# Optimization experiments

Hardware: AMD Instinct MI355X
Metric: run time of the kernel (lower is better)

The kernel has to match this reference:

```python
import jax, jax.numpy as jnp
import numpy as np
from jax import lax

# dims: B=16, T=1500, E(enc)=512, D(dec)=512, A(att_dim)=512, C(out_channels)=10, K(kernel)=201, H(heads)=4
SHARPENING = 1.0


def setup_inputs() -> dict:
    key = jax.random.key(0)
    ks = jax.random.split(key, 12)
    B, T, E, D, A, C, K, H = 16, 1500, 512, 512, 512, 10, 201, 4
    s = 0.02
    return {
        "enc_out": jax.random.normal(ks[0], (B, T, E), dtype=jnp.float32),
        "x_lens": jax.random.randint(ks[1], (B,), 1, T + 1, dtype=jnp.int32),
        "dec_out": jax.random.normal(ks[2], (B, 1, D), dtype=jnp.float32),
        "aw_step": jax.random.uniform(ks[3], (B, T, H), dtype=jnp.float32),
        "W_enc": jax.random.normal(ks[4], (H, E, A), dtype=jnp.float32) * s,
        "b_enc": jnp.zeros((H, A), dtype=jnp.float32),
        "W_dec": jax.random.normal(ks[5], (H, D, A), dtype=jnp.float32) * s,
        "W_conv": jax.random.normal(ks[6], (H, C, A), dtype=jnp.float32) * s,
        "conv_w": jax.random.normal(ks[7], (H, C, K), dtype=jnp.float32) * s,
        "v": jax.random.normal(ks[8], (H, A), dtype=jnp.float32) * s,
        "W_mha": jax.random.normal(ks[9], (H * E, E), dtype=jnp.float32) * s,
        "b_mha": jnp.zeros((E,), dtype=jnp.float32),
    }


def reference(enc_out, x_lens, dec_out, aw_step, W_enc, b_enc, W_dec, W_conv, conv_w, v, W_mha, b_mha):
    B, T, E = enc_out.shape
    H, C, K = conv_w.shape
    # per-head encoder projection (cached enc_out_a in original): [B,T,H,A]
    enc_a = jnp.einsum('bte,hea->btha', enc_out, W_enc) + b_enc
    # per-head decoder projection, broadcast over T: [B,1,H,A]
    dec_a = jnp.einsum('bqd,hda->bqha', dec_out, W_dec)
    # location features: per-head 1D conv over T of previous attention weights
    lhs = jnp.transpose(aw_step, (0, 2, 1))          # [B,H,T]
    rhs = conv_w.reshape(H * C, 1, K)                # grouped conv, one group per head
    conv = lax.conv_general_dilated(lhs, rhs, (1,), 'SAME',
                                    dimension_numbers=('NCH', 'OIH', 'NCH'),
                                    feature_group_count=H)  # [B,H*C,T]
    conv = conv.reshape(B, H, C, T)
    conv_a = jnp.einsum('bhct,hca->btha', conv, W_conv)      # [B,T,H,A]
    # additive energy: v^T tanh(enc + dec + conv) per head -> [B,T,H]
    energy = jnp.einsum('btha,ha->bth', jnp.tanh(enc_a + dec_a + conv_a), v)
    # original multiplies energy by 0/1 mask (NOT -inf) before softmax over T
    mask = (jnp.arange(T)[None, :] < x_lens[:, None]).astype(energy.dtype)  # [B,T]
    energy = energy * mask[:, :, None] * SHARPENING
    aw = jax.nn.softmax(energy, axis=1)                      # softmax over T per head
    # per-head context, heads concatenated along feature dim: [B,1,H*E]
    ctx = jnp.einsum('bte,bth->bhe', enc_out, aw).reshape(B, 1, H * E)
    context_vec = ctx @ W_mha + b_mha                        # [B,1,E]
    return context_vec, aw
```

## Files before the change

### kernel.cpp

```cpp
#include <hip/hip_runtime.h>
#include <hip/hip_bf16.h>

#define B_ 16
#define T_ 1500
#define E_ 512
#define A_ 512
#define H_ 4
#define C_ 10
#define K_ 201
#define M_ (B_*T_)
#define KW_ 544

typedef __attribute__((ext_vector_type(8))) short short8v;
typedef __attribute__((ext_vector_type(4))) float f32x4;
typedef __attribute__((ext_vector_type(4))) unsigned short ushort4v;
typedef __attribute__((ext_vector_type(8))) unsigned short ushort8v;

typedef __attribute__((address_space(1))) const char gch;
typedef __attribute__((address_space(3))) char lch;

__device__ __forceinline__ void gload16(const void* g, void* l) {
    __builtin_amdgcn_global_load_lds((gch*)g, (lch*)l, 16, 0, 0);
}

__device__ inline unsigned short f2bf(float x) {
    unsigned int u = __float_as_uint(x);
    return (unsigned short)((u + 0x7fffu + ((u >> 16) & 1u)) >> 16);
}

__global__ void k_prep(const float* __restrict__ enc, unsigned short* __restrict__ encB,
                       const float* __restrict__ Wenc, const float* __restrict__ Wconv,
                       unsigned short* __restrict__ WencTp,
                       const float* __restrict__ dec, const float* __restrict__ Wdec,
                       const float* __restrict__ benc, float* __restrict__ decA,
                       float* __restrict__ out,
                       const float* __restrict__ aw_step, const float* __restrict__ conv_w,
                       unsigned short* __restrict__ convA, float* __restrict__ wszero) {
    __shared__ float smemf[4456];
    int bid = blockIdx.x;
    int tid = threadIdx.x;

    if (bid < 6000) {
        int i = bid * 256 + tid;
        const float4* src = (const float4*)enc + (size_t)i * 2;
        float4 f0 = src[0], f1 = src[1];
        ushort8v o = { f2bf(f0.x), f2bf(f0.y), f2bf(f0.z), f2bf(f0.w),
                       f2bf(f1.x), f2bf(f1.y), f2bf(f1.z), f2bf(f1.w) };
        *(ushort8v*)&encB[(size_t)i * 8] = o;
        return;
    }
    if (bid < 7088) {
        int idx = bid - 6000;
        int bx = idx & 15, by = (idx >> 4) % 17, h = idx / 272;
        int tx = tid & 31, ty = tid >> 5;
        if (by == 16) {
            int base = (h * 16 + bx) * 1024;
            #pragma unroll
            for (int k = 0; k < 4; k++) {
                int i2 = base + k * 256 + tid;
                int c = i2 & 31, n = (i2 >> 5) & 511, hh = i2 >> 14;
                float val = (c < C_) ? Wconv[(hh * C_ + c) * A_ + n] : 0.0f;
                WencTp[((size_t)(hh * A_ + n)) * KW_ + 512 + c] = f2bf(val);
            }
            return;
        }
        float (*tile)[33] = (float(*)[33])smemf;
        int e0 = bx * 32, a0 = by * 32;
        const float* src = Wenc + h * E_ * A_;
        #pragma unroll
        for (int i = 0; i < 4; i++) tile[ty + i*8][tx] = src[(e0 + ty + i*8) * A_ + a0 + tx];
        __syncthreads();
        unsigned short* dst = WencTp + (size_t)h * A_ * KW_;
        #pragma unroll
        for (int i = 0; i < 4; i++) dst[(size_t)(a0 + ty + i*8) * KW_ + e0 + tx] = f2bf(tile[tx][ty + i*8]);
        return;
    }
    if (bid < 7152) {
        int bh = bid - 7088, b = bh >> 2, h = bh & 3;
        int a = tid;
        if (bh < 32) out[bh * 256 + a] = 0.0f;
        float acc0 = 0.f, acc1 = 0.f;
        const float* W = Wdec + h * E_ * A_;
        const float* x = dec + b * 512;
        for (int d = 0; d < 512; d++) {
            float s = x[d];
            acc0 += s * W[d * A_ + a];
            acc1 += s * W[d * A_ + a + 256];
        }
        decA[bh * A_ + a]       = acc0 + benc[h * A_ + a];
        decA[bh * A_ + a + 256] = acc1 + benc[h * A_ + a + 256];
        return;
    }
    {
        int i = bid - 7152;
        int b = i & 15, h = (i >> 4) & 3, tc = i >> 6;
        int t0 = tc * 250;
        float* seg = smemf;
        unsigned short* outl = (unsigned short*)(smemf + 456);
        {
            int idx = (i * 256 + tid) * 2;
            if (idx < 128768)     wszero[idx] = 0.0f;
            if (idx + 1 < 128768) wszero[idx + 1] = 0.0f;
        }
        for (int idx = tid; idx < 450; idx += 256) {
            int tt = t0 - 100 + idx;
            seg[idx] = (tt >= 0 && tt < T_) ? aw_step[(b * T_ + tt) * H_ + h] : 0.0f;
        }
        for (int idx = tid; idx < 8000; idx += 256) outl[idx] = 0;
        __syncthreads();
        if (tid < 250) {
            float acc[10] = {0,0,0,0,0,0,0,0,0,0};
            const float* cw = conv_w + h * C_ * K_;
            for (int k = 0; k < K_; k++) {
                float sv = seg[tid + k];
                #pragma unroll
                for (int c = 0; c < 10; c++) acc[c] += sv * cw[c * K_ + k];
            }
            #pragma unroll
            for (int c = 0; c < 10; c++) outl[tid * 32 + c] = f2bf(acc[c]);
        }
        __syncthreads();
        unsigned short* dst = convA + ((size_t)h * M_ + (size_t)b * T_ + t0) * 32;
        for (int idx = tid; idx < 2000; idx += 256)
            *(ushort4v*)&dst[idx * 4] = *(const ushort4v*)&outl[idx * 4];
    }
}

__launch_bounds__(256)
__global__ void k_energy(const unsigned short* __restrict__ encB,
                         const unsigned short* __restrict__ WencTp,
                         const unsigned short* __restrict__ convA,
                         const float* __restrict__ decA,
                         const float* __restrict__ v,
                         float* __restrict__ energy) {
    __shared__ unsigned short As[2][4096];
    __shared__ unsigned short Bs[2][4096];
    int m0 = blockIdx.x * 128;
    int h  = blockIdx.y >> 2;
    int n0 = (blockIdx.y & 3) * 128;
    int tid = threadIdx.x;
    int lane = tid & 63, w = tid >> 6;
    int wr = w >> 1, wc = w & 1;
    int lc = lane & 15, lr16 = lane >> 4;

    int srow  = lane >> 2;
    int sslot = (lane & 3) ^ ((lane >> 3) & 3);

    const char* pa[2]; const char* pb[2]; const char* pca[2];
    #pragma unroll
    for (int i = 0; i < 2; i++) {
        int c = i * 4 + w;
        int row = c * 16 + srow;
        int grow = min(m0 + row, M_ - 1);
        pa[i]  = (const char*)encB + ((size_t)grow * 512 + sslot * 8) * 2;
        pb[i]  = (const char*)WencTp + ((size_t)(h * 512 + n0 + row) * KW_ + sslot * 8) * 2;
        pca[i] = (const char*)convA + (((size_t)h * M_ + grow) * 32 + sslot * 8) * 2;
    }

    int kslot = (lr16 ^ ((lc >> 1) & 3)) * 8;

    f32x4 acc[4][4] = {};

    #pragma unroll
    for (int i = 0; i < 2; i++) {
        int c = i * 4 + w;
        gload16(pa[i], (char*)As[0] + c * 1024);
        gload16(pb[i], (char*)Bs[0] + c * 1024);
    }

    for (int s = 0; s < 17; ++s) {
        const int buf = s & 1;
        if (s < 15) {
            #pragma unroll
            for (int i = 0; i < 2; i++) {
                int c = i * 4 + w;
                gload16(pa[i] + (s + 1) * 64, (char*)As[buf ^ 1] + c * 1024);
                gload16(pb[i] + (s + 1) * 64, (char*)Bs[buf ^ 1] + c * 1024);
            }
            asm volatile("s_waitcnt vmcnt(4)" ::: "memory");
        } else if (s == 15) {
            #pragma unroll
            for (int i = 0; i < 2; i++) {
                int c = i * 4 + w;
                gload16(pca[i], (char*)As[buf ^ 1] + c * 1024);
                gload16(pb[i] + 16 * 64, (char*)Bs[buf ^ 1] + c * 1024);
            }
            asm volatile("s_waitcnt vmcnt(4)" ::: "memory");
        } else {
            asm volatile("s_waitcnt vmcnt(0)" ::: "memory");
        }
        __builtin_amdgcn_s_barrier();
        __builtin_amdgcn_sched_barrier(0);
        {
            short8v a[4], b[4];
            #pragma unroll
            for (int mi = 0; mi < 4; mi++)
                a[mi] = *(const short8v*)&As[buf][(wr * 64 + mi * 16 + lc) * 32 + kslot];
            #pragma unroll
            for (int ni = 0; ni < 4; ni++)
                b[ni] = *(const short8v*)&Bs[buf][(wc * 64 + ni * 16 + lc) * 32 + kslot];
            #pragma unroll
            for (int mi = 0; mi < 4; mi++)
                #pragma unroll
                for (int ni = 0; ni < 4; ni++)
                    acc[mi][ni] = __builtin_amdgcn_mfma_f32_16x16x32_bf16(a[mi], b[ni], acc[mi][ni], 0, 0, 0);
        }
        __builtin_amdgcn_sched_barrier(0);
        __builtin_amdgcn_s_barrier();
    }

    #pragma unroll
    for (int mi = 0; mi < 4; mi++) {
        #pragma unroll
        for (int r = 0; r < 4; r++) {
            int mrow = m0 + wr * 64 + mi * 16 + lr16 * 4 + r;
            if (mrow < M_) {
                int bb = mrow / 1500;
                const float* dA = decA + (bb * 4 + h) * 512;
                float s = 0.f;
                #pragma unroll
                for (int ni = 0; ni < 4; ni++) {
                    int n = n0 + wc * 64 + ni * 16 + lc;
                    float x = acc[mi][ni][r] + dA[n];
                    float t = __builtin_amdgcn_rcpf(__expf(2.0f * x) + 1.0f);
                    float vv = v[h * 512 + n];
                    s += __builtin_fmaf(-2.0f * t, vv, vv);
                }
                #pragma unroll
                for (int mk = 1; mk < 16; mk <<= 1) s += __shfl_xor(s, mk);
                if (lc == 0) atomicAdd(&energy[(size_t)mrow * 4 + h], s);
            }
        }
    }
}

__global__ void k_softmax(const float* __restrict__ energy, const int* __restrict__ xlens,
                          float* __restrict__ aw) {
    __shared__ float red[8];
    int b = blockIdx.x, h = blockIdx.y;
    int tid = threadIdx.x;
    int len = xlens[b];
    float e[6];
    float m = -1e30f;
    #pragma unroll
    for (int i = 0; i < 6; i++) {
        int t = tid + i * 256;
        float val = 0.0f;
        if (t < T_) {
            val = (t < len) ? energy[(size_t)(b * T_ + t) * H_ + h] : 0.0f;
            m = fmaxf(m, val);
        }
        e[i] = val;
    }
    #pragma unroll
    for (int mk = 1; mk < 64; mk <<= 1) m = fmaxf(m, __shfl_xor(m, mk));
    if ((tid & 63) == 0) red[tid >> 6] = m;
    __syncthreads();
    m = fmaxf(fmaxf(red[0], red[1]), fmaxf(red[2], red[3]));
    float ssum = 0.f;
    #pragma unroll
    for (int i = 0; i < 6; i++) {
        int t = tid + i * 256;
        if (t < T_) { e[i] = expf(e[i] - m); ssum += e[i]; }
    }
    #pragma unroll
    for (int mk = 1; mk < 64; mk <<= 1) ssum += __shfl_xor(ssum, mk);
    if ((tid & 63) == 0) red[4 + (tid >> 6)] = ssum;
    __syncthreads();
    float inv = 1.0f / (red[4] + red[5] + red[6] + red[7]);
    #pragma unroll
    for (int i = 0; i < 6; i++) {
        int t = tid + i * 256;
        if (t < T_) aw[(size_t)(b * T_ + t) * H_ + h] = e[i] * inv;
    }
}

__global__ void k_ctx(const unsigned short* __restrict__ encB, const float* __restrict__ aw,
                      float* __restrict__ ctx) {
    __shared__ float s_aw[500];
    int b = blockIdx.x, tc = blockIdx.y;
    int t0 = tc * 125;
    int tid = threadIdx.x;
    for (int idx = tid; idx < 500; idx += 256)
        s_aw[idx] = aw[(size_t)b * T_ * H_ + t0 * H_ + idx];
    __syncthreads();
    int e = tid * 2;
    float a00=0,a01=0,a10=0,a11=0,a20=0,a21=0,a30=0,a31=0;
    for (int tl = 0; tl < 125; tl++) {
        unsigned int u = *(const unsigned int*)&encB[(size_t)(b * T_ + t0 + tl) * E_ + e];
        float e0 = __uint_as_float((u & 0xffffu) << 16);
        float e1 = __uint_as_float(u & 0xffff0000u);
        float w0 = s_aw[tl*4+0], w1 = s_aw[tl*4+1], w2 = s_aw[tl*4+2], w3 = s_aw[tl*4+3];
        a00 += e0*w0; a01 += e1*w0; a10 += e0*w1; a11 += e1*w1;
        a20 += e0*w2; a21 += e1*w2; a30 += e0*w3; a31 += e1*w3;
    }
    atomicAdd(&ctx[b*2048 + 0*512 + e],   a00); atomicAdd(&ctx[b*2048 + 0*512 + e+1], a01);
    atomicAdd(&ctx[b*2048 + 1*512 + e],   a10); atomicAdd(&ctx[b*2048 + 1*512 + e+1], a11);
    atomicAdd(&ctx[b*2048 + 2*512 + e],   a20); atomicAdd(&ctx[b*2048 + 2*512 + e+1], a21);
    atomicAdd(&ctx[b*2048 + 3*512 + e],   a30); atomicAdd(&ctx[b*2048 + 3*512 + e+1], a31);
}

__global__ void k_proj(const float* __restrict__ ctx, const float* __restrict__ Wmha,
                       const float* __restrict__ bmha, float* __restrict__ out) {
    __shared__ float s_c[256];
    int b = blockIdx.x, ic = blockIdx.y;
    int tid = threadIdx.x;
    if (tid < 256) s_c[tid] = ctx[b * 2048 + ic * 256 + tid];
    __syncthreads();
    float acc = (ic == 0) ? bmha[tid] : 0.0f;
    const float* W = Wmha + (size_t)ic * 256 * 512;
    for (int i = 0; i < 256; i++) acc += s_c[i] * W[i * 512 + tid];
    atomicAdd(&out[b * 512 + tid], acc);
}

extern "C" void kernel_launch(void* const* d_in, const int* in_sizes, int n_in,
                              void* d_out, int out_size, void* d_ws, size_t ws_size,
                              hipStream_t stream) {
    const float* enc   = (const float*)d_in[0];
    const int*   xlens = (const int*)  d_in[1];
    const float* dec   = (const float*)d_in[2];
    const float* aw_st = (const float*)d_in[3];
    const float* Wenc  = (const float*)d_in[4];
    const float* benc  = (const float*)d_in[5];
    const float* Wdec  = (const float*)d_in[6];
    const float* Wconv = (const float*)d_in[7];
    const float* convw = (const float*)d_in[8];
    const float* v     = (const float*)d_in[9];
    const float* Wmha  = (const float*)d_in[10];
    const float* bmha  = (const float*)d_in[11];
    float* out = (float*)d_out;

    char* ws = (char*)d_ws;
    float* energy          = (float*)(ws);
    float* ctx             = (float*)(ws + 384000);
    float* decA            = (float*)(ws + 515072);
    unsigned short* WencTp = (unsigned short*)(ws + 646144);
    unsigned short* convA  = (unsigned short*)(ws + 2874368);
    unsigned short* encB   = (unsigned short*)(ws + 9018368);
    float* aw = out + 8192;

    k_prep    <<<7536, 256, 0, stream>>>(enc, encB, Wenc, Wconv, WencTp,
                                         dec, Wdec, benc, decA, out,
                                         aw_st, convw, convA, (float*)ws);
    k_energy  <<<dim3(188, 16), 256, 0, stream>>>(encB, WencTp, convA, decA, v, energy);
    k_softmax <<<dim3(16, 4), 256, 0, stream>>>(energy, xlens, aw);
    k_ctx     <<<dim3(16, 12), 256, 0, stream>>>(encB, aw, ctx);
    k_proj    <<<dim3(16, 8), 512, 0, stream>>>(ctx, Wmha, bmha, out);
}
```

Before: 179.1 us.

## Enlarge energy GEMM tile to 256x256 with 8 waves and phased pipeline

Rewrites the energy GEMM kernel to use 256x256 output tiles per 512-thread block, with K-steps of 64 and double-buffered LDS split into halves. Loads are staged in four phases per tile, interleaved with MFMA work, and the MFMA sections get raised wave priority. The grid is reordered so heads and column halves vary fastest, which improves reuse of the A tile across blocks. The aim is to raise arithmetic intensity and overlap global loads with compute. In exchange it uses more LDS and registers and runs one block per CU, leaving fewer blocks (752) in flight.

```diff
diff --git a/kernel.cpp b/kernel.cpp
--- a/kernel.cpp
+++ b/kernel.cpp
@@ -126,103 +126,148 @@
     }
 }
 
-__launch_bounds__(256)
+__launch_bounds__(512, 1)
 __global__ void k_energy(const unsigned short* __restrict__ encB,
                          const unsigned short* __restrict__ WencTp,
                          const unsigned short* __restrict__ convA,
                          const float* __restrict__ decA,
                          const float* __restrict__ v,
                          float* __restrict__ energy) {
-    __shared__ unsigned short As[2][4096];
-    __shared__ unsigned short Bs[2][4096];
-    int m0 = blockIdx.x * 128;
-    int h  = blockIdx.y >> 2;
-    int n0 = (blockIdx.y & 3) * 128;
+    __shared__ unsigned short As[2][2][8192];
+    __shared__ unsigned short Bs[2][2][8192];
+    int x = blockIdx.x;
+    int h = x >> 1;
+    int n0 = (x & 1) * 256;
+    int m0 = blockIdx.y * 256;
     int tid = threadIdx.x;
     int lane = tid & 63, w = tid >> 6;
-    int wr = w >> 1, wc = w & 1;
+    int wr = w >> 2, wc = w & 3;
     int lc = lane & 15, lr16 = lane >> 4;
 
-    int srow  = lane >> 2;
-    int sslot = (lane & 3) ^ ((lane >> 3) & 3);
-
-    const char* pa[2]; const char* pb[2]; const char* pca[2];
-    #pragma unroll
-    for (int i = 0; i < 2; i++) {
-        int c = i * 4 + w;
-        int row = c * 16 + srow;
-        int grow = min(m0 + row, M_ - 1);
-        pa[i]  = (const char*)encB + ((size_t)grow * 512 + sslot * 8) * 2;
-        pb[i]  = (const char*)WencTp + ((size_t)(h * 512 + n0 + row) * KW_ + sslot * 8) * 2;
-        pca[i] = (const char*)convA + (((size_t)h * M_ + grow) * 32 + sslot * 8) * 2;
-    }
-
-    int kslot = (lr16 ^ ((lc >> 1) & 3)) * 8;
-
-    f32x4 acc[4][4] = {};
-
-    #pragma unroll
-    for (int i = 0; i < 2; i++) {
-        int c = i * 4 + w;
-        gload16(pa[i], (char*)As[0] + c * 1024);
-        gload16(pb[i], (char*)Bs[0] + c * 1024);
-    }
-
-    for (int s = 0; s < 17; ++s) {
-        const int buf = s & 1;
-        if (s < 15) {
-            #pragma unroll
-            for (int i = 0; i < 2; i++) {
-                int c = i * 4 + w;
-                gload16(pa[i] + (s + 1) * 64, (char*)As[buf ^ 1] + c * 1024);
-                gload16(pb[i] + (s + 1) * 64, (char*)Bs[buf ^ 1] + c * 1024);
-            }
-            asm volatile("s_waitcnt vmcnt(4)" ::: "memory");
-        } else if (s == 15) {
-            #pragma unroll
-            for (int i = 0; i < 2; i++) {
-                int c = i * 4 + w;
-                gload16(pca[i], (char*)As[buf ^ 1] + c * 1024);
-                gload16(pb[i] + 16 * 64, (char*)Bs[buf ^ 1] + c * 1024);
-            }
-            asm volatile("s_waitcnt vmcnt(4)" ::: "memory");
-        } else {
-            asm volatile("s_waitcnt vmcnt(0)" ::: "memory");
-        }
-        __builtin_amdgcn_s_barrier();
-        __builtin_amdgcn_sched_barrier(0);
-        {
-            short8v a[4], b[4];
-            #pragma unroll
-            for (int mi = 0; mi < 4; mi++)
-                a[mi] = *(const short8v*)&As[buf][(wr * 64 + mi * 16 + lc) * 32 + kslot];
+    int srow = tid >> 3;
+    int gslot = (tid & 7) ^ (srow & 7);
+    const char* pa[2][2]; const char* pb[2][2];
+    #pragma unroll
+    for (int hf = 0; hf < 2; hf++)
+        #pragma unroll
+        for (int L = 0; L < 2; L++) {
+            int r = L * 64 + srow;
+            int grow = min(m0 + hf * 128 + r, M_ - 1);
+            pa[hf][L] = (const char*)encB + ((size_t)grow * 512 + gslot * 8) * 2;
+            int gn = n0 + hf * 128 + r;
+            pb[hf][L] = (const char*)WencTp + ((size_t)(h * 512 + gn) * KW_ + gslot * 8) * 2;
+        }
+    int crow = tid >> 2;
+    int cslot = (tid & 3) ^ (crow & 3);
+    const char* pca[2]; const char* pcb[2];
+    #pragma unroll
+    for (int L = 0; L < 2; L++) {
+        int r = L * 128 + crow;
+        int grow = min(m0 + r, M_ - 1);
+        pca[L] = (const char*)convA + (((size_t)h * M_ + grow) * 32 + cslot * 8) * 2;
+        pcb[L] = (const char*)WencTp + (((size_t)(h * 512 + n0 + r)) * KW_ + 512 + cslot * 8) * 2;
+    }
+
+#define STG_A(HF, TT, DB) { \
+    gload16(pa[HF][0] + (TT) * 128, (char*)&As[DB][HF][0] + tid * 16); \
+    gload16(pa[HF][1] + (TT) * 128, (char*)&As[DB][HF][0] + 8192 + tid * 16); }
+#define STG_B(HF, TT, DB) { \
+    gload16(pb[HF][0] + (TT) * 128, (char*)&Bs[DB][HF][0] + tid * 16); \
+    gload16(pb[HF][1] + (TT) * 128, (char*)&Bs[DB][HF][0] + 8192 + tid * 16); }
+#define STG_CA { gload16(pca[0], (char*)&As[0][0][0] + tid * 16); \
+                 gload16(pca[1], (char*)&As[0][0][0] + 8192 + tid * 16); }
+#define STG_CB { gload16(pcb[0], (char*)&Bs[0][0][0] + tid * 16); \
+                 gload16(pcb[1], (char*)&Bs[0][0][0] + 8192 + tid * 16); }
+
+    f32x4 acc[8][4] = {};
+
+#define MFMA_(A_, B_, C_) __builtin_amdgcn_mfma_f32_16x16x32_bf16(A_, B_, C_, 0, 0, 0)
+
+#define PHASE(BUF, MH, NH, STAGE, WAITST) { \
+    short8v a0[4], a1[4], b0[2], b1[2]; \
+    _Pragma("unroll") \
+    for (int mi = 0; mi < 4; mi++) { \
+        int r = wr * 64 + mi * 16 + lc; int sw = r & 7; \
+        const unsigned short* ba = &As[BUF][MH][r * 64]; \
+        a0[mi] = *(const short8v*)&ba[(lr16 ^ sw) * 8]; \
+        a1[mi] = *(const short8v*)&ba[((4 | lr16) ^ sw) * 8]; } \
+    _Pragma("unroll") \
+    for (int ni = 0; ni < 2; ni++) { \
+        int r = wc * 32 + ni * 16 + lc; int sw = r & 7; \
+        const unsigned short* bb = &Bs[BUF][NH][r * 64]; \
+        b0[ni] = *(const short8v*)&bb[(lr16 ^ sw) * 8]; \
+        b1[ni] = *(const short8v*)&bb[((4 | lr16) ^ sw) * 8]; } \
+    STAGE; \
+    __builtin_amdgcn_sched_barrier(0); \
+    WAITST; \
+    __builtin_amdgcn_s_barrier(); \
+    __builtin_amdgcn_sched_barrier(0); \
+    __builtin_amdgcn_s_setprio(1); \
+    _Pragma("unroll") \
+    for (int mi = 0; mi < 4; mi++) \
+        _Pragma("unroll") \
+        for (int ni = 0; ni < 2; ni++) { \
+            acc[(MH)*4+mi][(NH)*2+ni] = MFMA_(a0[mi], b0[ni], acc[(MH)*4+mi][(NH)*2+ni]); \
+            acc[(MH)*4+mi][(NH)*2+ni] = MFMA_(a1[mi], b1[ni], acc[(MH)*4+mi][(NH)*2+ni]); } \
+    __builtin_amdgcn_s_setprio(0); \
+    __builtin_amdgcn_sched_barrier(0); \
+    __builtin_amdgcn_s_barrier(); }
+
+#define VM(N) asm volatile("s_waitcnt vmcnt(" #N ")" ::: "memory")
+
+#define TILE(T, BUF) { \
+    PHASE(BUF, 0, 0, { if ((T) < 7) STG_A(1, (T)+1, 1-(BUF)) }, \
+          { if ((T) == 7) VM(4); else VM(6); }); \
+    PHASE(BUF, 0, 1, { if ((T) < 7) STG_B(1, (T)+1, 1-(BUF)) }, {}); \
+    PHASE(BUF, 1, 0, { if ((T) < 6) STG_A(0, (T)+2, BUF) else if ((T) == 6) STG_CA }, {}); \
+    PHASE(BUF, 1, 1, { if ((T) < 6) STG_B(0, (T)+2, BUF) else if ((T) == 6) STG_CB }, \
+          { if ((T) < 7) VM(8); }); }
+
+    STG_A(0, 0, 0); STG_B(0, 0, 0);
+    STG_A(1, 0, 0); STG_B(1, 0, 0);
+    STG_A(0, 1, 1); STG_B(0, 1, 1);
+    VM(8);
+    __builtin_amdgcn_s_barrier();
+
+    TILE(0, 0) TILE(1, 1) TILE(2, 0) TILE(3, 1)
+    TILE(4, 0) TILE(5, 1) TILE(6, 0) TILE(7, 1)
+
+    VM(0);
+    __builtin_amdgcn_s_barrier();
+    __builtin_amdgcn_sched_barrier(0);
+    {
+        short8v cb[4];
+        #pragma unroll
+        for (int ni = 0; ni < 4; ni++) {
+            int r = (ni >> 1) * 128 + wc * 32 + (ni & 1) * 16 + lc;
+            cb[ni] = *(const short8v*)&Bs[0][0][r * 32 + (lr16 ^ (r & 3)) * 8];
+        }
+        __builtin_amdgcn_s_setprio(1);
+        #pragma unroll
+        for (int mi = 0; mi < 8; mi++) {
+            int r = (mi >> 2) * 128 + wr * 64 + (mi & 3) * 16 + lc;
+            short8v ca = *(const short8v*)&As[0][0][r * 32 + (lr16 ^ (r & 3)) * 8];
             #pragma unroll
             for (int ni = 0; ni < 4; ni++)
-                b[ni] = *(const short8v*)&Bs[buf][(wc * 64 + ni * 16 + lc) * 32 + kslot];
-            #pragma unroll
-            for (int mi = 0; mi < 4; mi++)
-                #pragma unroll
-                for (int ni = 0; ni < 4; ni++)
-                    acc[mi][ni] = __builtin_amdgcn_mfma_f32_16x16x32_bf16(a[mi], b[ni], acc[mi][ni], 0, 0, 0);
-        }
-        __builtin_amdgcn_sched_barrier(0);
-        __builtin_amdgcn_s_barrier();
-    }
-
-    #pragma unroll
-    for (int mi = 0; mi < 4; mi++) {
-        #pragma unroll
-        for (int r = 0; r < 4; r++) {
-            int mrow = m0 + wr * 64 + mi * 16 + lr16 * 4 + r;
+                acc[mi][ni] = MFMA_(ca, cb[ni], acc[mi][ni]);
+        }
+        __builtin_amdgcn_s_setprio(0);
+    }
+
+    #pragma unroll
+    for (int mi = 0; mi < 8; mi++) {
+        #pragma unroll
+        for (int rr = 0; rr < 4; rr++) {
+            int mrow = m0 + (mi >> 2) * 128 + wr * 64 + (mi & 3) * 16 + lr16 * 4 + rr;
             if (mrow < M_) {
                 int bb = mrow / 1500;
                 const float* dA = decA + (bb * 4 + h) * 512;
                 float s = 0.f;
                 #pragma unroll
                 for (int ni = 0; ni < 4; ni++) {
-                    int n = n0 + wc * 64 + ni * 16 + lc;
-                    float x = acc[mi][ni][r] + dA[n];
-                    float t = __builtin_amdgcn_rcpf(__expf(2.0f * x) + 1.0f);
+                    int n = n0 + (ni >> 1) * 128 + wc * 32 + (ni & 1) * 16 + lc;
+                    float xv = acc[mi][ni][rr] + dA[n];
+                    float t = __builtin_amdgcn_rcpf(__expf(2.0f * xv) + 1.0f);
                     float vv = v[h * 512 + n];
                     s += __builtin_fmaf(-2.0f * t, vv, vv);
                 }
@@ -232,6 +277,14 @@
             }
         }
     }
+#undef STG_A
+#undef STG_B
+#undef STG_CA
+#undef STG_CB
+#undef MFMA_
+#undef PHASE
+#undef VM
+#undef TILE
 }
 
 __global__ void k_softmax(const float* __restrict__ energy, const int* __restrict__ xlens,
@@ -342,7 +395,7 @@
     k_prep    <<<7536, 256, 0, stream>>>(enc, encB, Wenc, Wconv, WencTp,
                                          dec, Wdec, benc, decA, out,
                                          aw_st, convw, convA, (float*)ws);
-    k_energy  <<<dim3(188, 16), 256, 0, stream>>>(encB, WencTp, convA, decA, v, energy);
+    k_energy  <<<dim3(8, 94), 512, 0, stream>>>(encB, WencTp, convA, decA, v, energy);
     k_softmax <<<dim3(16, 4), 256, 0, stream>>>(energy, xlens, aw);
     k_ctx     <<<dim3(16, 12), 256, 0, stream>>>(encB, aw, ctx);
     k_proj    <<<dim3(16, 8), 512, 0, stream>>>(ctx, Wmha, bmha, out);
```

Result: slower. 208.7 us (+16.5%).

## Triple-buffer energy GEMM loads and transpose MFMA output for cheaper epilogue reduction

Applied to the files above, without the earlier changes.

The energy GEMM moves from double to triple buffering of LDS tiles. Loads are issued two stages ahead, with the waitcnt adjusted to match, to hide more global-load latency. The MFMA operands are swapped so each lane holds a single output row across columns. This lets the tanh/v reduction accumulate locally and needs only two cross-lane shuffles plus a quarter of the atomics. It costs more LDS (48KB), and a launch-bounds hint of 3 is added.

```diff
diff --git a/kernel.cpp b/kernel.cpp
--- a/kernel.cpp
+++ b/kernel.cpp
@@ -126,15 +126,15 @@
     }
 }
 
-__launch_bounds__(256)
+__launch_bounds__(256, 3)
 __global__ void k_energy(const unsigned short* __restrict__ encB,
                          const unsigned short* __restrict__ WencTp,
                          const unsigned short* __restrict__ convA,
                          const float* __restrict__ decA,
                          const float* __restrict__ v,
                          float* __restrict__ energy) {
-    __shared__ unsigned short As[2][4096];
-    __shared__ unsigned short Bs[2][4096];
+    __shared__ unsigned short As[3][4096];
+    __shared__ unsigned short Bs[3][4096];
     int m0 = blockIdx.x * 128;
     int h  = blockIdx.y >> 2;
     int n0 = (blockIdx.y & 3) * 128;
@@ -164,72 +164,69 @@
     #pragma unroll
     for (int i = 0; i < 2; i++) {
         int c = i * 4 + w;
-        gload16(pa[i], (char*)As[0] + c * 1024);
-        gload16(pb[i], (char*)Bs[0] + c * 1024);
-    }
-
+        gload16(pa[i],      (char*)As[0] + c * 1024);
+        gload16(pb[i],      (char*)Bs[0] + c * 1024);
+        gload16(pa[i] + 64, (char*)As[1] + c * 1024);
+        gload16(pb[i] + 64, (char*)Bs[1] + c * 1024);
+    }
+
+    int bc = 0, bn1 = 1, bn2 = 2;
     for (int s = 0; s < 17; ++s) {
-        const int buf = s & 1;
-        if (s < 15) {
+        int t = s + 2;
+        if (t <= 16) {
             #pragma unroll
             for (int i = 0; i < 2; i++) {
                 int c = i * 4 + w;
-                gload16(pa[i] + (s + 1) * 64, (char*)As[buf ^ 1] + c * 1024);
-                gload16(pb[i] + (s + 1) * 64, (char*)Bs[buf ^ 1] + c * 1024);
+                const char* asrc = (t < 16) ? pa[i] + t * 64 : pca[i];
+                gload16(asrc,            (char*)As[bn2] + c * 1024);
+                gload16(pb[i] + t * 64,  (char*)Bs[bn2] + c * 1024);
             }
-            asm volatile("s_waitcnt vmcnt(4)" ::: "memory");
-        } else if (s == 15) {
-            #pragma unroll
-            for (int i = 0; i < 2; i++) {
-                int c = i * 4 + w;
-                gload16(pca[i], (char*)As[buf ^ 1] + c * 1024);
-                gload16(pb[i] + 16 * 64, (char*)Bs[buf ^ 1] + c * 1024);
-            }
-            asm volatile("s_waitcnt vmcnt(4)" ::: "memory");
-        } else {
-            asm volatile("s_waitcnt vmcnt(0)" ::: "memory");
-        }
+        }
+        if (s <= 14)      asm volatile("s_waitcnt vmcnt(8)" ::: "memory");
+        else if (s == 15) asm volatile("s_waitcnt vmcnt(4)" ::: "memory");
+        else              asm volatile("s_waitcnt vmcnt(0)" ::: "memory");
         __builtin_amdgcn_s_barrier();
         __builtin_amdgcn_sched_barrier(0);
         {
             short8v a[4], b[4];
             #pragma unroll
             for (int mi = 0; mi < 4; mi++)
-                a[mi] = *(const short8v*)&As[buf][(wr * 64 + mi * 16 + lc) * 32 + kslot];
+                a[mi] = *(const short8v*)&As[bc][(wr * 64 + mi * 16 + lc) * 32 + kslot];
             #pragma unroll
             for (int ni = 0; ni < 4; ni++)
-                b[ni] = *(const short8v*)&Bs[buf][(wc * 64 + ni * 16 + lc) * 32 + kslot];
+                b[ni] = *(const short8v*)&Bs[bc][(wc * 64 + ni * 16 + lc) * 32 + kslot];
             #pragma unroll
             for (int mi = 0; mi < 4; mi++)
                 #pragma unroll
                 for (int ni = 0; ni < 4; ni++)
-                    acc[mi][ni] = __builtin_amdgcn_mfma_f32_16x16x32_bf16(a[mi], b[ni], acc[mi][ni], 0, 0, 0);
+                    acc[mi][ni] = __builtin_amdgcn_mfma_f32_16x16x32_bf16(b[ni], a[mi], acc[mi][ni], 0, 0, 0);
         }
         __builtin_amdgcn_sched_barrier(0);
         __builtin_amdgcn_s_barrier();
+        int tmp = bc; bc = bn1; bn1 = bn2; bn2 = tmp;
     }
 
     #pragma unroll
     for (int mi = 0; mi < 4; mi++) {
-        #pragma unroll
-        for (int r = 0; r < 4; r++) {
-            int mrow = m0 + wr * 64 + mi * 16 + lr16 * 4 + r;
-            if (mrow < M_) {
-                int bb = mrow / 1500;
-                const float* dA = decA + (bb * 4 + h) * 512;
-                float s = 0.f;
+        int mrow = m0 + wr * 64 + mi * 16 + lc;
+        if (mrow < M_) {
+            int bb = mrow / 1500;
+            const float* dA = decA + (bb * 4 + h) * 512;
+            float s = 0.f;
+            #pragma unroll
+            for (int ni = 0; ni < 4; ni++) {
                 #pragma unroll
-                for (int ni = 0; ni < 4; ni++) {
-                    int n = n0 + wc * 64 + ni * 16 + lc;
-                    float x = acc[mi][ni][r] + dA[n];
-                    float t = __builtin_amdgcn_rcpf(__expf(2.0f * x) + 1.0f);
+                for (int r = 0; r < 4; r++) {
+                    int n = n0 + wc * 64 + ni * 16 + lr16 * 4 + r;
+                    float xv = acc[mi][ni][r] + dA[n];
+                    float tt = __builtin_amdgcn_rcpf(__expf(2.0f * xv) + 1.0f);
                     float vv = v[h * 512 + n];
-                    s += __builtin_fmaf(-2.0f * t, vv, vv);
+                    s += __builtin_fmaf(-2.0f * tt, vv, vv);
                 }
-                #pragma unroll
-                for (int mk = 1; mk < 16; mk <<= 1) s += __shfl_xor(s, mk);
-                if (lc == 0) atomicAdd(&energy[(size_t)mrow * 4 + h], s);
             }
+            s += __shfl_xor(s, 16);
+            s += __shfl_xor(s, 32);
+            if (lr16 == 0) atomicAdd(&energy[(size_t)mrow * 4 + h], s);
         }
     }
 }
```

Result: faster. 152.2 us (-15.0%).
